# Kernel optimization log

Measured on AMD Instinct MI355X. Metric: run time of the kernel, lower is better.

The kernel has to match this reference:

```python
import jax, jax.numpy as jnp
import numpy as np

E, TOP_K, H, I, GS, BITS = 32, 4, 2048, 1408, 128, 4
T = 1024
ROUTED_SCALE = 2.5
PACK = 32 // BITS  # 8 codes per int32


def _dequant(qpacked, qzeros, scales):
    """GPTQ-style dequant. qpacked: [O, C//8] int32 (8 x 4-bit codes per word),
    qzeros: [O, C//GS] int, scales: [O, C//GS] float -> W: [O, C] float."""
    shifts = (jnp.arange(PACK, dtype=jnp.int32) * BITS)
    codes = (qpacked[:, :, None] >> shifts[None, None, :]) & 0xF  # [O, C//8, 8]
    codes = codes.reshape(qpacked.shape[0], -1).astype(scales.dtype)  # [O, C]
    z = jnp.repeat(qzeros.astype(scales.dtype), GS, axis=-1)
    s = jnp.repeat(scales, GS, axis=-1)
    return (codes - z) * s


def setup_inputs() -> dict:
    key = jax.random.key(0)
    ks = jax.random.split(key, 16)
    d = {}
    d["hidden_states"] = jax.random.normal(ks[0], (T, H), jnp.float32)
    d["gate_w"] = jax.random.normal(ks[1], (H, E), jnp.float32) * 0.02
    # gate/up: out=I, in=H ; down: out=H, in=I
    d["gate_qweight"] = jax.random.randint(ks[2], (E, I, H // PACK), 0, 2147483647, jnp.int32)
    d["gate_qzeros"] = jax.random.randint(ks[3], (E, I, H // GS), 0, 16, jnp.int32)
    d["gate_scales"] = jax.random.uniform(ks[4], (E, I, H // GS), jnp.float32, 0.001, 0.01)
    d["up_qweight"] = jax.random.randint(ks[5], (E, I, H // PACK), 0, 2147483647, jnp.int32)
    d["up_qzeros"] = jax.random.randint(ks[6], (E, I, H // GS), 0, 16, jnp.int32)
    d["up_scales"] = jax.random.uniform(ks[7], (E, I, H // GS), jnp.float32, 0.001, 0.01)
    d["down_qweight"] = jax.random.randint(ks[8], (E, H, I // PACK), 0, 2147483647, jnp.int32)
    d["down_qzeros"] = jax.random.randint(ks[9], (E, H, I // GS), 0, 16, jnp.int32)
    d["down_scales"] = jax.random.uniform(ks[10], (E, H, I // GS), jnp.float32, 0.001, 0.01)
    ISH = 2 * I  # shared experts intermediate (n_shared_experts=2)
    d["shared_gate_w"] = jax.random.normal(ks[11], (H, ISH), jnp.float32) * 0.02
    d["shared_up_w"] = jax.random.normal(ks[12], (H, ISH), jnp.float32) * 0.02
    d["shared_down_w"] = jax.random.normal(ks[13], (ISH, H), jnp.float32) * 0.02
    return d


def _forward(hidden_states, gate_w, gate_qweight, gate_qzeros, gate_scales,
             up_qweight, up_qzeros, up_scales,
             down_qweight, down_qzeros, down_scales,
             shared_gate_w, shared_up_w, shared_down_w):
    x = hidden_states  # [T, H]
    t = x.shape[0]
    # ---- DeepSeek-V3 sigmoid router, top-k, renormalize, scale ----
    scores = jax.nn.sigmoid(x @ gate_w)  # [T, E]
    vals, idx = jax.lax.top_k(scores, TOP_K)  # [T, k]
    w = vals / (jnp.sum(vals, axis=-1, keepdims=True) + 1e-20) * ROUTED_SCALE
    # per-(token, expert) combine coefficient (sum over top-k slots)
    coeff = jnp.zeros((t, E), x.dtype).at[jnp.arange(t)[:, None], idx].add(w)  # [T, E]

    # ---- grouped dequant-GEMM over experts (scan keeps memory flat) ----
    def step(acc, p):
        Wg = _dequant(p["gq"], p["gz"], p["gs"])  # [I, H]
        Wu = _dequant(p["uq"], p["uz"], p["us"])  # [I, H]
        Wd = _dequant(p["dq"], p["dz"], p["ds"])  # [H, I]
        h = jax.nn.silu(x @ Wg.T) * (x @ Wu.T)    # [T, I]
        y = h @ Wd.T                              # [T, H]
        return acc + p["c"][:, None] * y, None

    xs = {"gq": gate_qweight, "gz": gate_qzeros, "gs": gate_scales,
          "uq": up_qweight, "uz": up_qzeros, "us": up_scales,
          "dq": down_qweight, "dz": down_qzeros, "ds": down_scales,
          "c": coeff.T}  # leading axis = expert
    moe_out, _ = jax.lax.scan(step, jnp.zeros_like(x), xs)

    # ---- shared experts (dense SwiGLU) on the residual stream ----
    shared = (jax.nn.silu(x @ shared_gate_w) * (x @ shared_up_w)) @ shared_down_w
    return moe_out + shared


def reference(hidden_states, gate_w, gate_qweight, gate_qzeros, gate_scales,
              up_qweight, up_qzeros, up_scales,
              down_qweight, down_qzeros, down_scales,
              shared_gate_w, shared_up_w, shared_down_w):
    return _forward(hidden_states, gate_w, gate_qweight, gate_qzeros, gate_scales,
                    up_qweight, up_qzeros, up_scales,
                    down_qweight, down_qzeros, down_scales,
                    shared_gate_w, shared_up_w, shared_down_w)
```

## Files before the change

kernel.cpp:

```cpp
#include <hip/hip_runtime.h>
#include <hip/hip_fp16.h>


#define T_TOK 1024
#define H_DIM 2048
#define I_DIM 1408
#define E_NUM 32
#define ISH   2816

typedef _Float16 f16_t;
typedef f16_t f16x8 __attribute__((ext_vector_type(8)));
typedef float f32x16 __attribute__((ext_vector_type(16)));

__device__ __forceinline__ uint32_t h2_u32(__half2 h) { union { __half2 h; uint32_t u; } c; c.h = h; return c.u; }
__device__ __forceinline__ __half2 u32_h2(uint32_t u) { union { uint32_t u; __half2 h; } c; c.u = u; return c.h; }

__device__ __forceinline__ uint32_t unpack_pair(uint32_t t, uint32_t z2, uint32_t s2) {
    uint32_t m = 0x64006400u | (t & 0xFu) | ((t & 0xF0u) << 12);
    __half2 h = __hsub2(u32_h2(m), u32_h2(z2));
    h = __hmul2(h, u32_h2(s2));
    return h2_u32(h);
}

__device__ __forceinline__ f16x8 unpack_frag(uint32_t w, uint32_t z2, uint32_t s2) {
    union { uint32_t u[4]; f16x8 v; } r;
    r.u[0] = unpack_pair(w, z2, s2);
    r.u[1] = unpack_pair(w >> 8, z2, s2);
    r.u[2] = unpack_pair(w >> 16, z2, s2);
    r.u[3] = unpack_pair(w >> 24, z2, s2);
    return r.v;
}

__device__ __forceinline__ int perm_routed(int u) { return ((u & 3) << 1) | ((u >> 2) & 1) | (u & 8); }
__device__ __forceinline__ int perm_shared(int u) { return ((u & 7) << 1) | (u >> 3); }

__device__ __forceinline__ float sigmoidf_(float v) { return 1.f / (1.f + __expf(-v)); }

__global__ __launch_bounds__(256)
void k_cvt(const float* __restrict__ in, __half* __restrict__ outp)
{
    const int i = blockIdx.x * 256 + threadIdx.x;
    const float4 a = *(const float4*)(in + (size_t)i * 8);
    const float4 b = *(const float4*)(in + (size_t)i * 8 + 4);
    int4 o;
    o.x = h2_u32(__floats2half2_rn(a.x, a.y));
    o.y = h2_u32(__floats2half2_rn(a.z, a.w));
    o.z = h2_u32(__floats2half2_rn(b.x, b.y));
    o.w = h2_u32(__floats2half2_rn(b.z, b.w));
    *(int4*)(outp + (size_t)i * 8) = o;
}

__global__ __launch_bounds__(256)
void k_tr(const float* __restrict__ in, __half* __restrict__ outp, int R, int C)
{
    __shared__ float tile[32][33];
    const int tx = threadIdx.x & 31, ty = threadIdx.x >> 5;
    const int cx = blockIdx.x * 32 + tx;
    #pragma unroll
    for (int j = 0; j < 4; ++j) {
        const int ry = blockIdx.y * 32 + ty + j * 8;
        tile[ty + j * 8][tx] = in[(size_t)ry * C + cx];
    }
    __syncthreads();
    const int ox = blockIdx.y * 32 + tx;
    #pragma unroll
    for (int j = 0; j < 4; ++j) {
        const int oy = blockIdx.x * 32 + ty + j * 8;
        outp[(size_t)oy * R + ox] = __float2half(tile[tx][ty + j * 8]);
    }
}

__global__ __launch_bounds__(256)
void k_router(const float* __restrict__ x, const float* __restrict__ gw,
              int* __restrict__ counts, int* __restrict__ elist, float* __restrict__ ecoef)
{
    const int t = blockIdx.x;
    const int tid = threadIdx.x;
    const int e = tid & 31, seg = tid >> 5;
    const float* xr = x + (size_t)t * H_DIM;
    float p = 0.f;
    for (int k = 0; k < 256; ++k)
        p = fmaf(xr[seg * 256 + k], gw[(seg * 256 + k) * E_NUM + e], p);
    __shared__ float ps[8][32];
    __shared__ float sc[32];
    ps[seg][e] = p;
    __syncthreads();
    if (tid < 32) {
        float s = 0.f;
        #pragma unroll
        for (int g = 0; g < 8; ++g) s += ps[g][tid];
        sc[tid] = sigmoidf_(s);
    }
    __syncthreads();
    if (tid == 0) {
        unsigned used = 0; float ssum = 0.f;
        int sel[4]; float sv[4];
        for (int k = 0; k < 4; ++k) {
            float best = -1.f; int bi = 0;
            for (int e2 = 0; e2 < 32; ++e2) {
                if (used & (1u << e2)) continue;
                if (sc[e2] > best) { best = sc[e2]; bi = e2; }
            }
            used |= 1u << bi; sel[k] = bi; sv[k] = best; ssum += best;
        }
        const float inv = 2.5f / (ssum + 1e-20f);
        for (int k = 0; k < 4; ++k) {
            const int ee = sel[k];
            const int pos = atomicAdd(&counts[ee], 1);
            elist[ee * T_TOK + pos] = t | (k << 20);
            ecoef[ee * T_TOK + pos] = sv[k] * inv;
        }
    }
}

__global__ __launch_bounds__(256)
void k_gateup(const __half* __restrict__ xq,
              const int* __restrict__ gqw, const int* __restrict__ gqz, const float* __restrict__ gsc,
              const int* __restrict__ uqw, const int* __restrict__ uqz, const float* __restrict__ usc,
              const int* __restrict__ counts, const int* __restrict__ elist, const float* __restrict__ ecoef,
              __half* __restrict__ h_buf)
{
    const int e = blockIdx.z;
    const int ne = counts[e];
    const int t0 = blockIdx.y * 64;
    if (t0 >= ne) return;
    const int tid = threadIdx.x;
    const int lane = tid & 63;
    const int wv = tid >> 6;
    const int li = lane & 31;
    const int c  = lane >> 5;
    const int i_col = blockIdx.x * 128 + wv * 32 + li;

    __shared__ int   toks[64];
    __shared__ float cofs[64];
    __shared__ __align__(16) char xs[64 * 256];

    if (tid < 64) {
        const bool v = (t0 + tid) < ne;
        toks[tid] = v ? elist[e * T_TOK + t0 + tid] : -1;
        cofs[tid] = v ? ecoef[e * T_TOK + t0 + tid] : 0.f;
    }

    f32x16 ag0, ag1, au0, au1;
    #pragma unroll
    for (int i = 0; i < 16; ++i) { ag0[i] = 0.f; ag1[i] = 0.f; au0[i] = 0.f; au1[i] = 0.f; }

    const size_t wrow = (size_t)(e * I_DIM + i_col);
    const int* gwr = gqw + wrow * 256;
    const int* uwr = uqw + wrow * 256;
    const int* gzr = gqz + wrow * 16;
    const int* uzr = uqz + wrow * 16;
    const float* gsr = gsc + wrow * 16;
    const float* usr = usc + wrow * 16;

    const int srow = tid >> 2;
    const int sq   = tid & 3;

    for (int g = 0; g < 16; ++g) {
        __syncthreads();
        {
            const int tk = toks[srow];
            const __half* src = (tk >= 0) ? (xq + (size_t)(tk & 0xFFFFF) * H_DIM + g * 128) : nullptr;
            #pragma unroll
            for (int cu = 0; cu < 4; ++cu) {
                const int u = sq * 4 + cu;
                int4 d = make_int4(0, 0, 0, 0);
                if (src) d = *(const int4*)(src + u * 8);
                *(int4*)(xs + srow * 256 + ((perm_routed(u) * 16) ^ ((srow & 7) << 4))) = d;
            }
        }
        __syncthreads();

        const int4 g1 = *(const int4*)(gwr + g * 16 + 4 * c);
        const int4 g2 = *(const int4*)(gwr + g * 16 + 8 + 4 * c);
        const int4 u1 = *(const int4*)(uwr + g * 16 + 4 * c);
        const int4 u2 = *(const int4*)(uwr + g * 16 + 8 + 4 * c);
        const uint32_t gz2 = 0x64006400u | ((uint32_t)gzr[g] * 0x10001u);
        const uint32_t uz2 = 0x64006400u | ((uint32_t)uzr[g] * 0x10001u);
        const uint32_t gs2 = h2_u32(__float2half2_rn(gsr[g]));
        const uint32_t us2 = h2_u32(__float2half2_rn(usr[g]));
        const uint32_t gwv[8] = {(uint32_t)g1.x,(uint32_t)g1.y,(uint32_t)g1.z,(uint32_t)g1.w,
                                 (uint32_t)g2.x,(uint32_t)g2.y,(uint32_t)g2.z,(uint32_t)g2.w};
        const uint32_t uwv[8] = {(uint32_t)u1.x,(uint32_t)u1.y,(uint32_t)u1.z,(uint32_t)u1.w,
                                 (uint32_t)u2.x,(uint32_t)u2.y,(uint32_t)u2.z,(uint32_t)u2.w};
        #pragma unroll
        for (int m = 0; m < 8; ++m) {
            const f16x8 bg = unpack_frag(gwv[m], gz2, gs2);
            const f16x8 bu = unpack_frag(uwv[m], uz2, us2);
            const int slotb = (2 * m + c) * 16;
            const f16x8 a0 = *(const f16x8*)(xs + li * 256 + (slotb ^ ((li & 7) << 4)));
            const f16x8 a1 = *(const f16x8*)(xs + (32 + li) * 256 + (slotb ^ ((li & 7) << 4)));
            ag0 = __builtin_amdgcn_mfma_f32_32x32x16_f16(a0, bg, ag0, 0, 0, 0);
            au0 = __builtin_amdgcn_mfma_f32_32x32x16_f16(a0, bu, au0, 0, 0, 0);
            ag1 = __builtin_amdgcn_mfma_f32_32x32x16_f16(a1, bg, ag1, 0, 0, 0);
            au1 = __builtin_amdgcn_mfma_f32_32x32x16_f16(a1, bu, au1, 0, 0, 0);
        }
    }

    #pragma unroll
    for (int r = 0; r < 16; ++r) {
        const int row0 = (r & 3) + 8 * (r >> 2) + 4 * c;
        {
            const int tk = toks[row0];
            if (tk >= 0) {
                const float gv = ag0[r], uv = au0[r];
                const float h = gv * sigmoidf_(gv) * uv * cofs[row0];
                h_buf[(size_t)((tk & 0xFFFFF) * 4 + (tk >> 20)) * I_DIM + i_col] = __float2half(h);
            }
        }
        {
            const int tk = toks[32 + row0];
            if (tk >= 0) {
                const float gv = ag1[r], uv = au1[r];
                const float h = gv * sigmoidf_(gv) * uv * cofs[32 + row0];
                h_buf[(size_t)((tk & 0xFFFFF) * 4 + (tk >> 20)) * I_DIM + i_col] = __float2half(h);
            }
        }
    }
}

__global__ __launch_bounds__(256)
void k_down(const __half* __restrict__ h_buf,
            const int* __restrict__ dqw, const int* __restrict__ dqz, const float* __restrict__ dsc,
            const int* __restrict__ counts, const int* __restrict__ elist,
            float* __restrict__ out)
{
    const int e = blockIdx.z;
    const int ne = counts[e];
    const int t0 = blockIdx.y * 64;
    if (t0 >= ne) return;
    const int tid = threadIdx.x;
    const int lane = tid & 63;
    const int wv = tid >> 6;
    const int li = lane & 31;
    const int c  = lane >> 5;
    const int h_col = blockIdx.x * 128 + wv * 32 + li;

    __shared__ int toks[64];
    __shared__ __align__(16) char xs[64 * 256];

    if (tid < 64) toks[tid] = ((t0 + tid) < ne) ? elist[e * T_TOK + t0 + tid] : -1;

    f32x16 a0, a1;
    #pragma unroll
    for (int i = 0; i < 16; ++i) { a0[i] = 0.f; a1[i] = 0.f; }

    const size_t wrow = (size_t)(e * H_DIM + h_col);
    const int* dwr = dqw + wrow * 176;
    const int* dzr = dqz + wrow * 11;
    const float* dsr = dsc + wrow * 11;

    const int srow = tid >> 2;
    const int sq   = tid & 3;

    for (int g = 0; g < 11; ++g) {
        __syncthreads();
        {
            const int tk = toks[srow];
            const __half* src = (tk >= 0)
                ? (h_buf + (size_t)((tk & 0xFFFFF) * 4 + (tk >> 20)) * I_DIM + g * 128) : nullptr;
            #pragma unroll
            for (int cu = 0; cu < 4; ++cu) {
                const int u = sq * 4 + cu;
                int4 d = make_int4(0, 0, 0, 0);
                if (src) d = *(const int4*)(src + u * 8);
                *(int4*)(xs + srow * 256 + ((perm_routed(u) * 16) ^ ((srow & 7) << 4))) = d;
            }
        }
        __syncthreads();

        const int4 w1 = *(const int4*)(dwr + g * 16 + 4 * c);
        const int4 w2 = *(const int4*)(dwr + g * 16 + 8 + 4 * c);
        const uint32_t z2 = 0x64006400u | ((uint32_t)dzr[g] * 0x10001u);
        const uint32_t s2 = h2_u32(__float2half2_rn(dsr[g]));
        const uint32_t wv8[8] = {(uint32_t)w1.x,(uint32_t)w1.y,(uint32_t)w1.z,(uint32_t)w1.w,
                                 (uint32_t)w2.x,(uint32_t)w2.y,(uint32_t)w2.z,(uint32_t)w2.w};
        #pragma unroll
        for (int m = 0; m < 8; ++m) {
            const f16x8 b = unpack_frag(wv8[m], z2, s2);
            const int slotb = (2 * m + c) * 16;
            const f16x8 x0 = *(const f16x8*)(xs + li * 256 + (slotb ^ ((li & 7) << 4)));
            const f16x8 x1 = *(const f16x8*)(xs + (32 + li) * 256 + (slotb ^ ((li & 7) << 4)));
            a0 = __builtin_amdgcn_mfma_f32_32x32x16_f16(x0, b, a0, 0, 0, 0);
            a1 = __builtin_amdgcn_mfma_f32_32x32x16_f16(x1, b, a1, 0, 0, 0);
        }
    }

    #pragma unroll
    for (int r = 0; r < 16; ++r) {
        const int row0 = (r & 3) + 8 * (r >> 2) + 4 * c;
        {
            const int tk = toks[row0];
            if (tk >= 0) atomicAdd(out + (size_t)(tk & 0xFFFFF) * H_DIM + h_col, a0[r]);
        }
        {
            const int tk = toks[32 + row0];
            if (tk >= 0) atomicAdd(out + (size_t)(tk & 0xFFFFF) * H_DIM + h_col, a1[r]);
        }
    }
}

__global__ __launch_bounds__(256)
void k_shared_gu(const __half* __restrict__ xq, const __half* __restrict__ wgt,
                 const __half* __restrict__ wut, __half* __restrict__ hs)
{
    const int t0 = blockIdx.y * 64;
    const int tid = threadIdx.x;
    const int lane = tid & 63;
    const int wv = tid >> 6;
    const int li = lane & 31;
    const int c  = lane >> 5;
    const int ncol = blockIdx.x * 128 + wv * 32 + li;

    __shared__ __align__(16) char xs[64 * 256];

    f32x16 ag0, ag1, au0, au1;
    #pragma unroll
    for (int i = 0; i < 16; ++i) { ag0[i] = 0.f; ag1[i] = 0.f; au0[i] = 0.f; au1[i] = 0.f; }

    const __half* gr = wgt + (size_t)ncol * H_DIM;
    const __half* ur = wut + (size_t)ncol * H_DIM;
    const int srow = tid >> 2;
    const int sq   = tid & 3;

    for (int g = 0; g < 16; ++g) {
        __syncthreads();
        {
            const __half* src = xq + (size_t)(t0 + srow) * H_DIM + g * 128;
            #pragma unroll
            for (int cu = 0; cu < 4; ++cu) {
                const int u = sq * 4 + cu;
                const int4 d = *(const int4*)(src + u * 8);
                *(int4*)(xs + srow * 256 + ((perm_shared(u) * 16) ^ ((srow & 7) << 4))) = d;
            }
        }
        __syncthreads();

        #pragma unroll
        for (int m = 0; m < 8; ++m) {
            const f16x8 bg = *(const f16x8*)(gr + g * 128 + c * 64 + m * 8);
            const f16x8 bu = *(const f16x8*)(ur + g * 128 + c * 64 + m * 8);
            const int slotb = (2 * m + c) * 16;
            const f16x8 a0 = *(const f16x8*)(xs + li * 256 + (slotb ^ ((li & 7) << 4)));
            const f16x8 a1 = *(const f16x8*)(xs + (32 + li) * 256 + (slotb ^ ((li & 7) << 4)));
            ag0 = __builtin_amdgcn_mfma_f32_32x32x16_f16(a0, bg, ag0, 0, 0, 0);
            au0 = __builtin_amdgcn_mfma_f32_32x32x16_f16(a0, bu, au0, 0, 0, 0);
            ag1 = __builtin_amdgcn_mfma_f32_32x32x16_f16(a1, bg, ag1, 0, 0, 0);
            au1 = __builtin_amdgcn_mfma_f32_32x32x16_f16(a1, bu, au1, 0, 0, 0);
        }
    }

    #pragma unroll
    for (int r = 0; r < 16; ++r) {
        const int row0 = (r & 3) + 8 * (r >> 2) + 4 * c;
        {
            const float gv = ag0[r], uv = au0[r];
            hs[(size_t)(t0 + row0) * ISH + ncol] = __float2half(gv * sigmoidf_(gv) * uv);
        }
        {
            const float gv = ag1[r], uv = au1[r];
            hs[(size_t)(t0 + 32 + row0) * ISH + ncol] = __float2half(gv * sigmoidf_(gv) * uv);
        }
    }
}

__global__ __launch_bounds__(256)
void k_shared_down(const __half* __restrict__ hs, const __half* __restrict__ wdt,
                   float* __restrict__ out)
{
    const int t0 = blockIdx.y * 64;
    const int tid = threadIdx.x;
    const int lane = tid & 63;
    const int wv = tid >> 6;
    const int li = lane & 31;
    const int c  = lane >> 5;
    const int hcol = blockIdx.x * 128 + wv * 32 + li;

    __shared__ __align__(16) char xs[64 * 256];

    f32x16 a0, a1;
    #pragma unroll
    for (int i = 0; i < 16; ++i) { a0[i] = 0.f; a1[i] = 0.f; }

    const __half* dr = wdt + (size_t)hcol * ISH;
    const int srow = tid >> 2;
    const int sq   = tid & 3;

    for (int g = 0; g < 22; ++g) {
        __syncthreads();
        {
            const __half* src = hs + (size_t)(t0 + srow) * ISH + g * 128;
            #pragma unroll
            for (int cu = 0; cu < 4; ++cu) {
                const int u = sq * 4 + cu;
                const int4 d = *(const int4*)(src + u * 8);
                *(int4*)(xs + srow * 256 + ((perm_shared(u) * 16) ^ ((srow & 7) << 4))) = d;
            }
        }
        __syncthreads();

        #pragma unroll
        for (int m = 0; m < 8; ++m) {
            const f16x8 b = *(const f16x8*)(dr + g * 128 + c * 64 + m * 8);
            const int slotb = (2 * m + c) * 16;
            const f16x8 x0 = *(const f16x8*)(xs + li * 256 + (slotb ^ ((li & 7) << 4)));
            const f16x8 x1 = *(const f16x8*)(xs + (32 + li) * 256 + (slotb ^ ((li & 7) << 4)));
            a0 = __builtin_amdgcn_mfma_f32_32x32x16_f16(x0, b, a0, 0, 0, 0);
            a1 = __builtin_amdgcn_mfma_f32_32x32x16_f16(x1, b, a1, 0, 0, 0);
        }
    }

    #pragma unroll
    for (int r = 0; r < 16; ++r) {
        const int row0 = (r & 3) + 8 * (r >> 2) + 4 * c;
        out[(size_t)(t0 + row0) * H_DIM + hcol] = a0[r];
        out[(size_t)(t0 + 32 + row0) * H_DIM + hcol] = a1[r];
    }
}

extern "C" void kernel_launch(void* const* d_in, const int* in_sizes, int n_in,
                              void* d_out, int out_size, void* d_ws, size_t ws_size,
                              hipStream_t stream)
{
    const float* x   = (const float*)d_in[0];
    const float* gw  = (const float*)d_in[1];
    const int*   gqw = (const int*)d_in[2];
    const int*   gqz = (const int*)d_in[3];
    const float* gsc = (const float*)d_in[4];
    const int*   uqw = (const int*)d_in[5];
    const int*   uqz = (const int*)d_in[6];
    const float* usc = (const float*)d_in[7];
    const int*   dqw = (const int*)d_in[8];
    const int*   dqz = (const int*)d_in[9];
    const float* dsc = (const float*)d_in[10];
    const float* sgw = (const float*)d_in[11];
    const float* suw = (const float*)d_in[12];
    const float* sdw = (const float*)d_in[13];
    float* out = (float*)d_out;

    char* ws = (char*)d_ws;
    constexpr size_t OFF_COUNTS = 0;
    constexpr size_t OFF_ELIST  = 1024;
    constexpr size_t OFF_ECOEF  = OFF_ELIST + (size_t)E_NUM * T_TOK * 4;
    constexpr size_t OFF_XQ     = OFF_ECOEF + (size_t)E_NUM * T_TOK * 4;
    constexpr size_t OFF_WGT    = OFF_XQ + (size_t)T_TOK * H_DIM * 2;
    constexpr size_t OFF_WUT    = OFF_WGT + (size_t)ISH * H_DIM * 2;
    constexpr size_t OFF_WDT    = OFF_WUT + (size_t)ISH * H_DIM * 2;
    constexpr size_t OFF_HBUF   = OFF_WDT + (size_t)H_DIM * ISH * 2;
    constexpr size_t OFF_HS     = OFF_HBUF + (size_t)T_TOK * 4 * I_DIM * 2;

    int*    counts = (int*)(ws + OFF_COUNTS);
    int*    elist  = (int*)(ws + OFF_ELIST);
    float*  ecoef  = (float*)(ws + OFF_ECOEF);
    __half* xq     = (__half*)(ws + OFF_XQ);
    __half* wgt    = (__half*)(ws + OFF_WGT);
    __half* wut    = (__half*)(ws + OFF_WUT);
    __half* wdt    = (__half*)(ws + OFF_WDT);
    __half* h_buf  = (__half*)(ws + OFF_HBUF);
    __half* hs     = (__half*)(ws + OFF_HS);

    hipMemsetAsync(counts, 0, E_NUM * sizeof(int), stream);
    k_cvt<<<dim3((T_TOK * H_DIM / 8) / 256), 256, 0, stream>>>(x, xq);
    k_tr<<<dim3(ISH / 32, H_DIM / 32), 256, 0, stream>>>(sgw, wgt, H_DIM, ISH);
    k_tr<<<dim3(ISH / 32, H_DIM / 32), 256, 0, stream>>>(suw, wut, H_DIM, ISH);
    k_tr<<<dim3(H_DIM / 32, ISH / 32), 256, 0, stream>>>(sdw, wdt, ISH, H_DIM);
    k_router<<<dim3(T_TOK), 256, 0, stream>>>(x, gw, counts, elist, ecoef);
    k_gateup<<<dim3(I_DIM / 128, T_TOK / 64, E_NUM), 256, 0, stream>>>(
        xq, gqw, gqz, gsc, uqw, uqz, usc, counts, elist, ecoef, h_buf);
    k_shared_gu<<<dim3(ISH / 128, T_TOK / 64), 256, 0, stream>>>(xq, wgt, wut, hs);
    k_shared_down<<<dim3(H_DIM / 128, T_TOK / 64), 256, 0, stream>>>(hs, wdt, out);
    k_down<<<dim3(H_DIM / 128, T_TOK / 64, E_NUM), 256, 0, stream>>>(
        h_buf, dqw, dqz, dsc, counts, elist, out);
}
```

Baseline: 636.4 us.

## Double-buffer LDS staging via global_load_lds and double token tile per block

Replaces the register-staged, swizzled LDS fill in all four GEMM kernels with direct global-to-LDS 16-byte loads into a slot-major layout. The LDS buffer is doubled and quantized weight loads are prefetched one group ahead, so data movement overlaps with MFMA work. Blocks grow to 512 threads covering 128 tokens, which halves how often each weight tile is fetched. A zeroed workspace row stands in for padding tokens. The cost is more LDS per block, which may lower occupancy, and more idle work in expert tiles that are only partly filled.

```diff
diff --git a/kernel.cpp b/kernel.cpp
--- a/kernel.cpp
+++ b/kernel.cpp
@@ -12,8 +12,13 @@
 typedef f16_t f16x8 __attribute__((ext_vector_type(8)));
 typedef float f32x16 __attribute__((ext_vector_type(16)));
 
-__device__ __forceinline__ uint32_t h2_u32(__half2 h) { union { __half2 h; uint32_t u; } c; c.h = h; return c.u; }
-__device__ __forceinline__ __half2 u32_h2(uint32_t u) { union { uint32_t u; __half2 h; } c; c.u = u; return c.h; }
+__device__ __forceinline__ uint32_t h2_u32(__half2 h){union{__half2 h;uint32_t u;}c;c.h=h;return c.u;}
+__device__ __forceinline__ __half2 u32_h2(uint32_t u){union{uint32_t u;__half2 h;}c;c.u=u;return c.h;}
+
+__device__ __forceinline__ void glds16(const void* g, void* l) {
+    __builtin_amdgcn_global_load_lds((const __attribute__((address_space(1))) void*)g,
+                                     (__attribute__((address_space(3))) void*)l, 16, 0, 0);
+}
 
 __device__ __forceinline__ uint32_t unpack_pair(uint32_t t, uint32_t z2, uint32_t s2) {
     uint32_t m = 0x64006400u | (t & 0xFu) | ((t & 0xF0u) << 12);
@@ -21,7 +26,6 @@
     h = __hmul2(h, u32_h2(s2));
     return h2_u32(h);
 }
-
 __device__ __forceinline__ f16x8 unpack_frag(uint32_t w, uint32_t z2, uint32_t s2) {
     union { uint32_t u[4]; f16x8 v; } r;
     r.u[0] = unpack_pair(w, z2, s2);
@@ -30,9 +34,7 @@
     r.u[3] = unpack_pair(w >> 24, z2, s2);
     return r.v;
 }
-
-__device__ __forceinline__ int perm_routed(int u) { return ((u & 3) << 1) | ((u >> 2) & 1) | (u & 8); }
-__device__ __forceinline__ int perm_shared(int u) { return ((u & 7) << 1) | (u >> 3); }
+__device__ __forceinline__ int invp(int s) { return ((s >> 1) & 3) | ((s & 1) << 2) | (s & 8); }
 
 __device__ __forceinline__ float sigmoidf_(float v) { return 1.f / (1.f + __expf(-v)); }
 
@@ -57,17 +59,13 @@
     const int tx = threadIdx.x & 31, ty = threadIdx.x >> 5;
     const int cx = blockIdx.x * 32 + tx;
     #pragma unroll
-    for (int j = 0; j < 4; ++j) {
-        const int ry = blockIdx.y * 32 + ty + j * 8;
-        tile[ty + j * 8][tx] = in[(size_t)ry * C + cx];
-    }
+    for (int j = 0; j < 4; ++j)
+        tile[ty + j * 8][tx] = in[(size_t)(blockIdx.y * 32 + ty + j * 8) * C + cx];
     __syncthreads();
     const int ox = blockIdx.y * 32 + tx;
     #pragma unroll
-    for (int j = 0; j < 4; ++j) {
-        const int oy = blockIdx.x * 32 + ty + j * 8;
-        outp[(size_t)oy * R + ox] = __float2half(tile[tx][ty + j * 8]);
-    }
+    for (int j = 0; j < 4; ++j)
+        outp[(size_t)(blockIdx.x * 32 + ty + j * 8) * R + ox] = __float2half(tile[tx][ty + j * 8]);
 }
 
 __global__ __launch_bounds__(256)
@@ -113,37 +111,54 @@
     }
 }
 
-__global__ __launch_bounds__(256)
+struct GUW { int4 g1, g2, u1, u2; int gz, uz; float gs, us; };
+__device__ __forceinline__ GUW gu_wload(const int* gwr, const int* uwr, const int* gzr,
+                                        const int* uzr, const float* gsr, const float* usr,
+                                        int g, int c) {
+    GUW w;
+    w.g1 = *(const int4*)(gwr + g * 16 + 4 * c);
+    w.g2 = *(const int4*)(gwr + g * 16 + 8 + 4 * c);
+    w.u1 = *(const int4*)(uwr + g * 16 + 4 * c);
+    w.u2 = *(const int4*)(uwr + g * 16 + 8 + 4 * c);
+    w.gz = gzr[g]; w.uz = uzr[g]; w.gs = gsr[g]; w.us = usr[g];
+    return w;
+}
+
+__global__ __launch_bounds__(512)
 void k_gateup(const __half* __restrict__ xq,
               const int* __restrict__ gqw, const int* __restrict__ gqz, const float* __restrict__ gsc,
               const int* __restrict__ uqw, const int* __restrict__ uqz, const float* __restrict__ usc,
               const int* __restrict__ counts, const int* __restrict__ elist, const float* __restrict__ ecoef,
-              __half* __restrict__ h_buf)
+              const __half* __restrict__ zrow, __half* __restrict__ h_buf)
 {
     const int e = blockIdx.z;
     const int ne = counts[e];
-    const int t0 = blockIdx.y * 64;
+    const int t0 = blockIdx.y * 128;
     if (t0 >= ne) return;
     const int tid = threadIdx.x;
     const int lane = tid & 63;
     const int wv = tid >> 6;
     const int li = lane & 31;
-    const int c  = lane >> 5;
-    const int i_col = blockIdx.x * 128 + wv * 32 + li;
-
-    __shared__ int   toks[64];
-    __shared__ float cofs[64];
-    __shared__ __align__(16) char xs[64 * 256];
-
-    if (tid < 64) {
+    const int c = lane >> 5;
+    const int ng = wv & 3, th = wv >> 2;
+    const int i_col = blockIdx.x * 128 + ng * 32 + li;
+
+    __shared__ int toks[128];
+    __shared__ float cofs[128];
+    __shared__ __align__(16) char xs[2][16 * 2048];
+
+    if (tid < 128) {
         const bool v = (t0 + tid) < ne;
         toks[tid] = v ? elist[e * T_TOK + t0 + tid] : -1;
         cofs[tid] = v ? ecoef[e * T_TOK + t0 + tid] : 0.f;
     }
-
-    f32x16 ag0, ag1, au0, au1;
-    #pragma unroll
-    for (int i = 0; i < 16; ++i) { ag0[i] = 0.f; ag1[i] = 0.f; au0[i] = 0.f; au1[i] = 0.f; }
+    __syncthreads();
+
+    const int tk0 = toks[lane], tk1 = toks[64 + lane];
+    const __half* sr0 = (tk0 >= 0) ? xq + (size_t)(tk0 & 0xFFFFF) * H_DIM : zrow;
+    const __half* sr1 = (tk1 >= 0) ? xq + (size_t)(tk1 & 0xFFFFF) * H_DIM : zrow;
+    const int s0 = wv * 2, s1 = wv * 2 + 1;
+    const int u0 = invp(s0), u1 = invp(s1);
 
     const size_t wrow = (size_t)(e * I_DIM + i_col);
     const int* gwr = gqw + wrow * 256;
@@ -153,136 +168,167 @@
     const float* gsr = gsc + wrow * 16;
     const float* usr = usc + wrow * 16;
 
-    const int srow = tid >> 2;
-    const int sq   = tid & 3;
-
-    for (int g = 0; g < 16; ++g) {
-        __syncthreads();
-        {
-            const int tk = toks[srow];
-            const __half* src = (tk >= 0) ? (xq + (size_t)(tk & 0xFFFFF) * H_DIM + g * 128) : nullptr;
-            #pragma unroll
-            for (int cu = 0; cu < 4; ++cu) {
-                const int u = sq * 4 + cu;
-                int4 d = make_int4(0, 0, 0, 0);
-                if (src) d = *(const int4*)(src + u * 8);
-                *(int4*)(xs + srow * 256 + ((perm_routed(u) * 16) ^ ((srow & 7) << 4))) = d;
-            }
-        }
-        __syncthreads();
-
-        const int4 g1 = *(const int4*)(gwr + g * 16 + 4 * c);
-        const int4 g2 = *(const int4*)(gwr + g * 16 + 8 + 4 * c);
-        const int4 u1 = *(const int4*)(uwr + g * 16 + 4 * c);
-        const int4 u2 = *(const int4*)(uwr + g * 16 + 8 + 4 * c);
-        const uint32_t gz2 = 0x64006400u | ((uint32_t)gzr[g] * 0x10001u);
-        const uint32_t uz2 = 0x64006400u | ((uint32_t)uzr[g] * 0x10001u);
-        const uint32_t gs2 = h2_u32(__float2half2_rn(gsr[g]));
-        const uint32_t us2 = h2_u32(__float2half2_rn(usr[g]));
-        const uint32_t gwv[8] = {(uint32_t)g1.x,(uint32_t)g1.y,(uint32_t)g1.z,(uint32_t)g1.w,
-                                 (uint32_t)g2.x,(uint32_t)g2.y,(uint32_t)g2.z,(uint32_t)g2.w};
-        const uint32_t uwv[8] = {(uint32_t)u1.x,(uint32_t)u1.y,(uint32_t)u1.z,(uint32_t)u1.w,
-                                 (uint32_t)u2.x,(uint32_t)u2.y,(uint32_t)u2.z,(uint32_t)u2.w};
-        #pragma unroll
-        for (int m = 0; m < 8; ++m) {
-            const f16x8 bg = unpack_frag(gwv[m], gz2, gs2);
-            const f16x8 bu = unpack_frag(uwv[m], uz2, us2);
-            const int slotb = (2 * m + c) * 16;
-            const f16x8 a0 = *(const f16x8*)(xs + li * 256 + (slotb ^ ((li & 7) << 4)));
-            const f16x8 a1 = *(const f16x8*)(xs + (32 + li) * 256 + (slotb ^ ((li & 7) << 4)));
-            ag0 = __builtin_amdgcn_mfma_f32_32x32x16_f16(a0, bg, ag0, 0, 0, 0);
-            au0 = __builtin_amdgcn_mfma_f32_32x32x16_f16(a0, bu, au0, 0, 0, 0);
-            ag1 = __builtin_amdgcn_mfma_f32_32x32x16_f16(a1, bg, ag1, 0, 0, 0);
-            au1 = __builtin_amdgcn_mfma_f32_32x32x16_f16(a1, bu, au1, 0, 0, 0);
-        }
+    f32x16 ag0, ag1, au0, au1;
+    #pragma unroll
+    for (int i = 0; i < 16; ++i) { ag0[i] = 0.f; ag1[i] = 0.f; au0[i] = 0.f; au1[i] = 0.f; }
+
+#define GU_STAGE(B, g) do { \
+    glds16(sr0 + (g) * 128 + u0 * 8, xs[B] + s0 * 2048); \
+    glds16(sr1 + (g) * 128 + u0 * 8, xs[B] + s0 * 2048 + 1024); \
+    glds16(sr0 + (g) * 128 + u1 * 8, xs[B] + s1 * 2048); \
+    glds16(sr1 + (g) * 128 + u1 * 8, xs[B] + s1 * 2048 + 1024); } while (0)
+
+#define GU_COMP(B, W) do { \
+    const uint32_t gz2 = 0x64006400u | ((uint32_t)(W).gz * 0x10001u); \
+    const uint32_t uz2 = 0x64006400u | ((uint32_t)(W).uz * 0x10001u); \
+    const uint32_t gs2 = h2_u32(__float2half2_rn((W).gs)); \
+    const uint32_t us2 = h2_u32(__float2half2_rn((W).us)); \
+    const uint32_t gw8[8] = {(uint32_t)(W).g1.x,(uint32_t)(W).g1.y,(uint32_t)(W).g1.z,(uint32_t)(W).g1.w, \
+                             (uint32_t)(W).g2.x,(uint32_t)(W).g2.y,(uint32_t)(W).g2.z,(uint32_t)(W).g2.w}; \
+    const uint32_t uw8[8] = {(uint32_t)(W).u1.x,(uint32_t)(W).u1.y,(uint32_t)(W).u1.z,(uint32_t)(W).u1.w, \
+                             (uint32_t)(W).u2.x,(uint32_t)(W).u2.y,(uint32_t)(W).u2.z,(uint32_t)(W).u2.w}; \
+    _Pragma("unroll") \
+    for (int m = 0; m < 8; ++m) { \
+        const f16x8 bg = unpack_frag(gw8[m], gz2, gs2); \
+        const f16x8 bu = unpack_frag(uw8[m], uz2, us2); \
+        const char* ap = xs[B] + (2 * m + c) * 2048 + (th * 64 + li) * 16; \
+        const f16x8 a0 = *(const f16x8*)ap; \
+        const f16x8 a1 = *(const f16x8*)(ap + 512); \
+        ag0 = __builtin_amdgcn_mfma_f32_32x32x16_f16(a0, bg, ag0, 0, 0, 0); \
+        au0 = __builtin_amdgcn_mfma_f32_32x32x16_f16(a0, bu, au0, 0, 0, 0); \
+        ag1 = __builtin_amdgcn_mfma_f32_32x32x16_f16(a1, bg, ag1, 0, 0, 0); \
+        au1 = __builtin_amdgcn_mfma_f32_32x32x16_f16(a1, bu, au1, 0, 0, 0); \
+    } } while (0)
+
+    GUW W0 = gu_wload(gwr, uwr, gzr, uzr, gsr, usr, 0, c), W1;
+    GU_STAGE(0, 0);
+    __syncthreads();
+    for (int g = 0; g < 16; g += 2) {
+        GU_STAGE(1, g + 1);
+        W1 = gu_wload(gwr, uwr, gzr, uzr, gsr, usr, g + 1, c);
+        GU_COMP(0, W0);
+        __syncthreads();
+        if (g + 2 < 16) {
+            GU_STAGE(0, g + 2);
+            W0 = gu_wload(gwr, uwr, gzr, uzr, gsr, usr, g + 2, c);
+        }
+        GU_COMP(1, W1);
+        __syncthreads();
     }
 
     #pragma unroll
     for (int r = 0; r < 16; ++r) {
         const int row0 = (r & 3) + 8 * (r >> 2) + 4 * c;
         {
-            const int tk = toks[row0];
+            const int rr = th * 64 + row0;
+            const int tk = toks[rr];
             if (tk >= 0) {
                 const float gv = ag0[r], uv = au0[r];
-                const float h = gv * sigmoidf_(gv) * uv * cofs[row0];
-                h_buf[(size_t)((tk & 0xFFFFF) * 4 + (tk >> 20)) * I_DIM + i_col] = __float2half(h);
+                h_buf[(size_t)((tk & 0xFFFFF) * 4 + (tk >> 20)) * I_DIM + i_col] =
+                    __float2half(gv * sigmoidf_(gv) * uv * cofs[rr]);
             }
         }
         {
-            const int tk = toks[32 + row0];
+            const int rr = th * 64 + 32 + row0;
+            const int tk = toks[rr];
             if (tk >= 0) {
                 const float gv = ag1[r], uv = au1[r];
-                const float h = gv * sigmoidf_(gv) * uv * cofs[32 + row0];
-                h_buf[(size_t)((tk & 0xFFFFF) * 4 + (tk >> 20)) * I_DIM + i_col] = __float2half(h);
+                h_buf[(size_t)((tk & 0xFFFFF) * 4 + (tk >> 20)) * I_DIM + i_col] =
+                    __float2half(gv * sigmoidf_(gv) * uv * cofs[rr]);
             }
         }
     }
-}
-
-__global__ __launch_bounds__(256)
+#undef GU_STAGE
+#undef GU_COMP
+}
+
+struct DW { int4 w1, w2; int z; float s; };
+__device__ __forceinline__ DW d_wload(const int* dwr, const int* dzr, const float* dsr, int g, int c) {
+    DW w;
+    w.w1 = *(const int4*)(dwr + g * 16 + 4 * c);
+    w.w2 = *(const int4*)(dwr + g * 16 + 8 + 4 * c);
+    w.z = dzr[g]; w.s = dsr[g];
+    return w;
+}
+
+__global__ __launch_bounds__(512)
 void k_down(const __half* __restrict__ h_buf,
             const int* __restrict__ dqw, const int* __restrict__ dqz, const float* __restrict__ dsc,
             const int* __restrict__ counts, const int* __restrict__ elist,
-            float* __restrict__ out)
+            const __half* __restrict__ zrow, float* __restrict__ out)
 {
     const int e = blockIdx.z;
     const int ne = counts[e];
-    const int t0 = blockIdx.y * 64;
+    const int t0 = blockIdx.y * 128;
     if (t0 >= ne) return;
     const int tid = threadIdx.x;
     const int lane = tid & 63;
     const int wv = tid >> 6;
     const int li = lane & 31;
-    const int c  = lane >> 5;
-    const int h_col = blockIdx.x * 128 + wv * 32 + li;
-
-    __shared__ int toks[64];
-    __shared__ __align__(16) char xs[64 * 256];
-
-    if (tid < 64) toks[tid] = ((t0 + tid) < ne) ? elist[e * T_TOK + t0 + tid] : -1;
-
-    f32x16 a0, a1;
-    #pragma unroll
-    for (int i = 0; i < 16; ++i) { a0[i] = 0.f; a1[i] = 0.f; }
+    const int c = lane >> 5;
+    const int ng = wv & 3, th = wv >> 2;
+    const int h_col = blockIdx.x * 128 + ng * 32 + li;
+
+    __shared__ int toks[128];
+    __shared__ __align__(16) char xs[2][16 * 2048];
+
+    if (tid < 128)
+        toks[tid] = ((t0 + tid) < ne) ? elist[e * T_TOK + t0 + tid] : -1;
+    __syncthreads();
+
+    const int tk0 = toks[lane], tk1 = toks[64 + lane];
+    const __half* sr0 = (tk0 >= 0) ? h_buf + (size_t)((tk0 & 0xFFFFF) * 4 + (tk0 >> 20)) * I_DIM : zrow;
+    const __half* sr1 = (tk1 >= 0) ? h_buf + (size_t)((tk1 & 0xFFFFF) * 4 + (tk1 >> 20)) * I_DIM : zrow;
+    const int s0 = wv * 2, s1 = wv * 2 + 1;
+    const int u0 = invp(s0), u1 = invp(s1);
 
     const size_t wrow = (size_t)(e * H_DIM + h_col);
     const int* dwr = dqw + wrow * 176;
     const int* dzr = dqz + wrow * 11;
     const float* dsr = dsc + wrow * 11;
 
-    const int srow = tid >> 2;
-    const int sq   = tid & 3;
-
-    for (int g = 0; g < 11; ++g) {
-        __syncthreads();
-        {
-            const int tk = toks[srow];
-            const __half* src = (tk >= 0)
-                ? (h_buf + (size_t)((tk & 0xFFFFF) * 4 + (tk >> 20)) * I_DIM + g * 128) : nullptr;
-            #pragma unroll
-            for (int cu = 0; cu < 4; ++cu) {
-                const int u = sq * 4 + cu;
-                int4 d = make_int4(0, 0, 0, 0);
-                if (src) d = *(const int4*)(src + u * 8);
-                *(int4*)(xs + srow * 256 + ((perm_routed(u) * 16) ^ ((srow & 7) << 4))) = d;
+    f32x16 a0, a1;
+    #pragma unroll
+    for (int i = 0; i < 16; ++i) { a0[i] = 0.f; a1[i] = 0.f; }
+
+#define D_STAGE(B, g) do { \
+    glds16(sr0 + (g) * 128 + u0 * 8, xs[B] + s0 * 2048); \
+    glds16(sr1 + (g) * 128 + u0 * 8, xs[B] + s0 * 2048 + 1024); \
+    glds16(sr0 + (g) * 128 + u1 * 8, xs[B] + s1 * 2048); \
+    glds16(sr1 + (g) * 128 + u1 * 8, xs[B] + s1 * 2048 + 1024); } while (0)
+
+#define D_COMP(B, W) do { \
+    const uint32_t z2 = 0x64006400u | ((uint32_t)(W).z * 0x10001u); \
+    const uint32_t s2 = h2_u32(__float2half2_rn((W).s)); \
+    const uint32_t w8[8] = {(uint32_t)(W).w1.x,(uint32_t)(W).w1.y,(uint32_t)(W).w1.z,(uint32_t)(W).w1.w, \
+                            (uint32_t)(W).w2.x,(uint32_t)(W).w2.y,(uint32_t)(W).w2.z,(uint32_t)(W).w2.w}; \
+    _Pragma("unroll") \
+    for (int m = 0; m < 8; ++m) { \
+        const f16x8 b = unpack_frag(w8[m], z2, s2); \
+        const char* ap = xs[B] + (2 * m + c) * 2048 + (th * 64 + li) * 16; \
+        const f16x8 x0 = *(const f16x8*)ap; \
+        const f16x8 x1 = *(const f16x8*)(ap + 512); \
+        a0 = __builtin_amdgcn_mfma_f32_32x32x16_f16(x0, b, a0, 0, 0, 0); \
+        a1 = __builtin_amdgcn_mfma_f32_32x32x16_f16(x1, b, a1, 0, 0, 0); \
+    } } while (0)
+
+    DW W0 = d_wload(dwr, dzr, dsr, 0, c), W1;
+    D_STAGE(0, 0);
+    __syncthreads();
+    for (int g = 0; g < 11; g += 2) {
+        if (g + 1 < 11) {
+            D_STAGE(1, g + 1);
+            W1 = d_wload(dwr, dzr, dsr, g + 1, c);
+        }
+        D_COMP(0, W0);
+        __syncthreads();
+        if (g + 1 < 11) {
+            if (g + 2 < 11) {
+                D_STAGE(0, g + 2);
+                W0 = d_wload(dwr, dzr, dsr, g + 2, c);
             }
-        }
-        __syncthreads();
-
-        const int4 w1 = *(const int4*)(dwr + g * 16 + 4 * c);
-        const int4 w2 = *(const int4*)(dwr + g * 16 + 8 + 4 * c);
-        const uint32_t z2 = 0x64006400u | ((uint32_t)dzr[g] * 0x10001u);
-        const uint32_t s2 = h2_u32(__float2half2_rn(dsr[g]));
-        const uint32_t wv8[8] = {(uint32_t)w1.x,(uint32_t)w1.y,(uint32_t)w1.z,(uint32_t)w1.w,
-                                 (uint32_t)w2.x,(uint32_t)w2.y,(uint32_t)w2.z,(uint32_t)w2.w};
-        #pragma unroll
-        for (int m = 0; m < 8; ++m) {
-            const f16x8 b = unpack_frag(wv8[m], z2, s2);
-            const int slotb = (2 * m + c) * 16;
-            const f16x8 x0 = *(const f16x8*)(xs + li * 256 + (slotb ^ ((li & 7) << 4)));
-            const f16x8 x1 = *(const f16x8*)(xs + (32 + li) * 256 + (slotb ^ ((li & 7) << 4)));
-            a0 = __builtin_amdgcn_mfma_f32_32x32x16_f16(x0, b, a0, 0, 0, 0);
-            a1 = __builtin_amdgcn_mfma_f32_32x32x16_f16(x1, b, a1, 0, 0, 0);
+            D_COMP(1, W1);
+            __syncthreads();
         }
     }
 
@@ -290,64 +336,80 @@
     for (int r = 0; r < 16; ++r) {
         const int row0 = (r & 3) + 8 * (r >> 2) + 4 * c;
         {
-            const int tk = toks[row0];
+            const int tk = toks[th * 64 + row0];
             if (tk >= 0) atomicAdd(out + (size_t)(tk & 0xFFFFF) * H_DIM + h_col, a0[r]);
         }
         {
-            const int tk = toks[32 + row0];
+            const int tk = toks[th * 64 + 32 + row0];
             if (tk >= 0) atomicAdd(out + (size_t)(tk & 0xFFFFF) * H_DIM + h_col, a1[r]);
         }
     }
-}
-
-__global__ __launch_bounds__(256)
+#undef D_STAGE
+#undef D_COMP
+}
+
+__global__ __launch_bounds__(512)
 void k_shared_gu(const __half* __restrict__ xq, const __half* __restrict__ wgt,
                  const __half* __restrict__ wut, __half* __restrict__ hs)
 {
-    const int t0 = blockIdx.y * 64;
+    const int t0 = blockIdx.y * 128;
+    const int nb = blockIdx.x * 128;
     const int tid = threadIdx.x;
     const int lane = tid & 63;
     const int wv = tid >> 6;
     const int li = lane & 31;
-    const int c  = lane >> 5;
-    const int ncol = blockIdx.x * 128 + wv * 32 + li;
-
-    __shared__ __align__(16) char xs[64 * 256];
+    const int c = lane >> 5;
+    const int ng = wv & 3, th = wv >> 2;
+    const int ncol = nb + ng * 32 + li;
+
+    __shared__ __align__(16) char xa[2][8 * 2048];
+    __shared__ __align__(16) char bg[2][8 * 2048];
+    __shared__ __align__(16) char bu[2][8 * 2048];
+
+    const __half* ar0 = xq + (size_t)(t0 + lane) * H_DIM;
+    const __half* ar1 = xq + (size_t)(t0 + 64 + lane) * H_DIM;
+    const __half* gr0 = wgt + (size_t)(nb + lane) * H_DIM;
+    const __half* gr1 = wgt + (size_t)(nb + 64 + lane) * H_DIM;
+    const __half* ur0 = wut + (size_t)(nb + lane) * H_DIM;
+    const __half* ur1 = wut + (size_t)(nb + 64 + lane) * H_DIM;
 
     f32x16 ag0, ag1, au0, au1;
     #pragma unroll
     for (int i = 0; i < 16; ++i) { ag0[i] = 0.f; ag1[i] = 0.f; au0[i] = 0.f; au1[i] = 0.f; }
 
-    const __half* gr = wgt + (size_t)ncol * H_DIM;
-    const __half* ur = wut + (size_t)ncol * H_DIM;
-    const int srow = tid >> 2;
-    const int sq   = tid & 3;
-
-    for (int g = 0; g < 16; ++g) {
-        __syncthreads();
-        {
-            const __half* src = xq + (size_t)(t0 + srow) * H_DIM + g * 128;
-            #pragma unroll
-            for (int cu = 0; cu < 4; ++cu) {
-                const int u = sq * 4 + cu;
-                const int4 d = *(const int4*)(src + u * 8);
-                *(int4*)(xs + srow * 256 + ((perm_shared(u) * 16) ^ ((srow & 7) << 4))) = d;
-            }
-        }
-        __syncthreads();
-
-        #pragma unroll
-        for (int m = 0; m < 8; ++m) {
-            const f16x8 bg = *(const f16x8*)(gr + g * 128 + c * 64 + m * 8);
-            const f16x8 bu = *(const f16x8*)(ur + g * 128 + c * 64 + m * 8);
-            const int slotb = (2 * m + c) * 16;
-            const f16x8 a0 = *(const f16x8*)(xs + li * 256 + (slotb ^ ((li & 7) << 4)));
-            const f16x8 a1 = *(const f16x8*)(xs + (32 + li) * 256 + (slotb ^ ((li & 7) << 4)));
-            ag0 = __builtin_amdgcn_mfma_f32_32x32x16_f16(a0, bg, ag0, 0, 0, 0);
-            au0 = __builtin_amdgcn_mfma_f32_32x32x16_f16(a0, bu, au0, 0, 0, 0);
-            ag1 = __builtin_amdgcn_mfma_f32_32x32x16_f16(a1, bg, ag1, 0, 0, 0);
-            au1 = __builtin_amdgcn_mfma_f32_32x32x16_f16(a1, bu, au1, 0, 0, 0);
-        }
+#define SG_STAGE(B, g) do { \
+    const int off = (g) * 64 + wv * 8; \
+    glds16(ar0 + off, xa[B] + wv * 2048); \
+    glds16(ar1 + off, xa[B] + wv * 2048 + 1024); \
+    glds16(gr0 + off, bg[B] + wv * 2048); \
+    glds16(gr1 + off, bg[B] + wv * 2048 + 1024); \
+    glds16(ur0 + off, bu[B] + wv * 2048); \
+    glds16(ur1 + off, bu[B] + wv * 2048 + 1024); } while (0)
+
+#define SG_COMP(B) do { \
+    _Pragma("unroll") \
+    for (int m = 0; m < 4; ++m) { \
+        const int so = (2 * m + c) * 2048; \
+        const char* ap = xa[B] + so + (th * 64 + li) * 16; \
+        const f16x8 a0 = *(const f16x8*)ap; \
+        const f16x8 a1 = *(const f16x8*)(ap + 512); \
+        const f16x8 wg = *(const f16x8*)(bg[B] + so + (ng * 32 + li) * 16); \
+        const f16x8 wu = *(const f16x8*)(bu[B] + so + (ng * 32 + li) * 16); \
+        ag0 = __builtin_amdgcn_mfma_f32_32x32x16_f16(a0, wg, ag0, 0, 0, 0); \
+        au0 = __builtin_amdgcn_mfma_f32_32x32x16_f16(a0, wu, au0, 0, 0, 0); \
+        ag1 = __builtin_amdgcn_mfma_f32_32x32x16_f16(a1, wg, ag1, 0, 0, 0); \
+        au1 = __builtin_amdgcn_mfma_f32_32x32x16_f16(a1, wu, au1, 0, 0, 0); \
+    } } while (0)
+
+    SG_STAGE(0, 0);
+    __syncthreads();
+    for (int g = 0; g < 32; g += 2) {
+        SG_STAGE(1, g + 1);
+        SG_COMP(0);
+        __syncthreads();
+        if (g + 2 < 32) SG_STAGE(0, g + 2);
+        SG_COMP(1);
+        __syncthreads();
     }
 
     #pragma unroll
@@ -355,67 +417,81 @@
         const int row0 = (r & 3) + 8 * (r >> 2) + 4 * c;
         {
             const float gv = ag0[r], uv = au0[r];
-            hs[(size_t)(t0 + row0) * ISH + ncol] = __float2half(gv * sigmoidf_(gv) * uv);
+            hs[(size_t)(t0 + th * 64 + row0) * ISH + ncol] = __float2half(gv * sigmoidf_(gv) * uv);
         }
         {
             const float gv = ag1[r], uv = au1[r];
-            hs[(size_t)(t0 + 32 + row0) * ISH + ncol] = __float2half(gv * sigmoidf_(gv) * uv);
-        }
-    }
-}
-
-__global__ __launch_bounds__(256)
+            hs[(size_t)(t0 + th * 64 + 32 + row0) * ISH + ncol] = __float2half(gv * sigmoidf_(gv) * uv);
+        }
+    }
+#undef SG_STAGE
+#undef SG_COMP
+}
+
+__global__ __launch_bounds__(512)
 void k_shared_down(const __half* __restrict__ hs, const __half* __restrict__ wdt,
                    float* __restrict__ out)
 {
-    const int t0 = blockIdx.y * 64;
+    const int t0 = blockIdx.y * 128;
+    const int hb = blockIdx.x * 128;
     const int tid = threadIdx.x;
     const int lane = tid & 63;
     const int wv = tid >> 6;
     const int li = lane & 31;
-    const int c  = lane >> 5;
-    const int hcol = blockIdx.x * 128 + wv * 32 + li;
-
-    __shared__ __align__(16) char xs[64 * 256];
+    const int c = lane >> 5;
+    const int ng = wv & 3, th = wv >> 2;
+    const int hcol = hb + ng * 32 + li;
+
+    __shared__ __align__(16) char xa[2][8 * 2048];
+    __shared__ __align__(16) char bd[2][8 * 2048];
+
+    const __half* ar0 = hs + (size_t)(t0 + lane) * ISH;
+    const __half* ar1 = hs + (size_t)(t0 + 64 + lane) * ISH;
+    const __half* dr0 = wdt + (size_t)(hb + lane) * ISH;
+    const __half* dr1 = wdt + (size_t)(hb + 64 + lane) * ISH;
 
     f32x16 a0, a1;
     #pragma unroll
     for (int i = 0; i < 16; ++i) { a0[i] = 0.f; a1[i] = 0.f; }
 
-    const __half* dr = wdt + (size_t)hcol * ISH;
-    const int srow = tid >> 2;
-    const int sq   = tid & 3;
-
-    for (int g = 0; g < 22; ++g) {
-        __syncthreads();
-        {
-            const __half* src = hs + (size_t)(t0 + srow) * ISH + g * 128;
-            #pragma unroll
-            for (int cu = 0; cu < 4; ++cu) {
-                const int u = sq * 4 + cu;
-                const int4 d = *(const int4*)(src + u * 8);
-                *(int4*)(xs + srow * 256 + ((perm_shared(u) * 16) ^ ((srow & 7) << 4))) = d;
-            }
-        }
-        __syncthreads();
-
-        #pragma unroll
-        for (int m = 0; m < 8; ++m) {
-            const f16x8 b = *(const f16x8*)(dr + g * 128 + c * 64 + m * 8);
-            const int slotb = (2 * m + c) * 16;
-            const f16x8 x0 = *(const f16x8*)(xs + li * 256 + (slotb ^ ((li & 7) << 4)));
-            const f16x8 x1 = *(const f16x8*)(xs + (32 + li) * 256 + (slotb ^ ((li & 7) << 4)));
-            a0 = __builtin_amdgcn_mfma_f32_32x32x16_f16(x0, b, a0, 0, 0, 0);
-            a1 = __builtin_amdgcn_mfma_f32_32x32x16_f16(x1, b, a1, 0, 0, 0);
-        }
+#define SD_STAGE(B, g) do { \
+    const int off = (g) * 64 + wv * 8; \
+    glds16(ar0 + off, xa[B] + wv * 2048); \
+    glds16(ar1 + off, xa[B] + wv * 2048 + 1024); \
+    glds16(dr0 + off, bd[B] + wv * 2048); \
+    glds16(dr1 + off, bd[B] + wv * 2048 + 1024); } while (0)
+
+#define SD_COMP(B) do { \
+    _Pragma("unroll") \
+    for (int m = 0; m < 4; ++m) { \
+        const int so = (2 * m + c) * 2048; \
+        const char* ap = xa[B] + so + (th * 64 + li) * 16; \
+        const f16x8 x0 = *(const f16x8*)ap; \
+        const f16x8 x1 = *(const f16x8*)(ap + 512); \
+        const f16x8 wd = *(const f16x8*)(bd[B] + so + (ng * 32 + li) * 16); \
+        a0 = __builtin_amdgcn_mfma_f32_32x32x16_f16(x0, wd, a0, 0, 0, 0); \
+        a1 = __builtin_amdgcn_mfma_f32_32x32x16_f16(x1, wd, a1, 0, 0, 0); \
+    } } while (0)
+
+    SD_STAGE(0, 0);
+    __syncthreads();
+    for (int g = 0; g < 44; g += 2) {
+        SD_STAGE(1, g + 1);
+        SD_COMP(0);
+        __syncthreads();
+        if (g + 2 < 44) SD_STAGE(0, g + 2);
+        SD_COMP(1);
+        __syncthreads();
     }
 
     #pragma unroll
     for (int r = 0; r < 16; ++r) {
         const int row0 = (r & 3) + 8 * (r >> 2) + 4 * c;
-        out[(size_t)(t0 + row0) * H_DIM + hcol] = a0[r];
-        out[(size_t)(t0 + 32 + row0) * H_DIM + hcol] = a1[r];
-    }
+        out[(size_t)(t0 + th * 64 + row0) * H_DIM + hcol] = a0[r];
+        out[(size_t)(t0 + th * 64 + 32 + row0) * H_DIM + hcol] = a1[r];
+    }
+#undef SD_STAGE
+#undef SD_COMP
 }
 
 extern "C" void kernel_launch(void* const* d_in, const int* in_sizes, int n_in,
@@ -440,7 +516,8 @@
 
     char* ws = (char*)d_ws;
     constexpr size_t OFF_COUNTS = 0;
-    constexpr size_t OFF_ELIST  = 1024;
+    constexpr size_t OFF_ZERO   = 1024;
+    constexpr size_t OFF_ELIST  = OFF_ZERO + 8192;
     constexpr size_t OFF_ECOEF  = OFF_ELIST + (size_t)E_NUM * T_TOK * 4;
     constexpr size_t OFF_XQ     = OFF_ECOEF + (size_t)E_NUM * T_TOK * 4;
     constexpr size_t OFF_WGT    = OFF_XQ + (size_t)T_TOK * H_DIM * 2;
@@ -450,6 +527,7 @@
     constexpr size_t OFF_HS     = OFF_HBUF + (size_t)T_TOK * 4 * I_DIM * 2;
 
     int*    counts = (int*)(ws + OFF_COUNTS);
+    __half* zrow   = (__half*)(ws + OFF_ZERO);
     int*    elist  = (int*)(ws + OFF_ELIST);
     float*  ecoef  = (float*)(ws + OFF_ECOEF);
     __half* xq     = (__half*)(ws + OFF_XQ);
@@ -459,16 +537,16 @@
     __half* h_buf  = (__half*)(ws + OFF_HBUF);
     __half* hs     = (__half*)(ws + OFF_HS);
 
-    hipMemsetAsync(counts, 0, E_NUM * sizeof(int), stream);
+    hipMemsetAsync(ws, 0, OFF_ZERO + 8192, stream);
     k_cvt<<<dim3((T_TOK * H_DIM / 8) / 256), 256, 0, stream>>>(x, xq);
     k_tr<<<dim3(ISH / 32, H_DIM / 32), 256, 0, stream>>>(sgw, wgt, H_DIM, ISH);
     k_tr<<<dim3(ISH / 32, H_DIM / 32), 256, 0, stream>>>(suw, wut, H_DIM, ISH);
     k_tr<<<dim3(H_DIM / 32, ISH / 32), 256, 0, stream>>>(sdw, wdt, ISH, H_DIM);
     k_router<<<dim3(T_TOK), 256, 0, stream>>>(x, gw, counts, elist, ecoef);
-    k_gateup<<<dim3(I_DIM / 128, T_TOK / 64, E_NUM), 256, 0, stream>>>(
-        xq, gqw, gqz, gsc, uqw, uqz, usc, counts, elist, ecoef, h_buf);
-    k_shared_gu<<<dim3(ISH / 128, T_TOK / 64), 256, 0, stream>>>(xq, wgt, wut, hs);
-    k_shared_down<<<dim3(H_DIM / 128, T_TOK / 64), 256, 0, stream>>>(hs, wdt, out);
-    k_down<<<dim3(H_DIM / 128, T_TOK / 64, E_NUM), 256, 0, stream>>>(
-        h_buf, dqw, dqz, dsc, counts, elist, out);
-}
+    k_gateup<<<dim3(I_DIM / 128, T_TOK / 128, E_NUM), 512, 0, stream>>>(
+        xq, gqw, gqz, gsc, uqw, uqz, usc, counts, elist, ecoef, zrow, h_buf);
+    k_shared_gu<<<dim3(ISH / 128, T_TOK / 128), 512, 0, stream>>>(xq, wgt, wut, hs);
+    k_shared_down<<<dim3(H_DIM / 128, T_TOK / 128), 512, 0, stream>>>(hs, wdt, out);
+    k_down<<<dim3(H_DIM / 128, T_TOK / 128, E_NUM), 512, 0, stream>>>(
+        h_buf, dqw, dqz, dsc, counts, elist, zrow, out);
+}
```

Result: slower. 707.0 us (+11.1%).
